# Kernel optimization log

Hardware: AMD Instinct MI355X
Metric: run time of the kernel (lower is better)

## Reference

```python
import jax, jax.numpy as jnp
import numpy as np

B, T, I, H = 64, 512, 1024, 2048


def setup_inputs() -> dict:
    key = jax.random.key(0)
    ks = jax.random.split(key, 6)
    s = 1.0 / np.sqrt(H).astype(np.float32)
    return {
        "input": jax.random.normal(ks[0], (B, T, I), jnp.float32),
        "internal": jax.random.normal(ks[1], (B, T), jnp.float32) * 0.1,
        "w_ih": jax.random.uniform(ks[2], (H, I), jnp.float32, -s, s),
        "w_hh": jax.random.uniform(ks[3], (H, H), jnp.float32, -s, s),
        "b_ih": jax.random.uniform(ks[4], (H,), jnp.float32, -s, s),
        "b_hh": jax.random.uniform(ks[5], (H,), jnp.float32, -s, s),
        "h0": jnp.zeros((1, B, H), jnp.float32),
        "trunc": 64,
    }


def reference(input, internal, w_ih, w_hh, b_ih, b_hh, h0, trunc):
    # input: [B, T, I]; internal: [B, T] scalar-per-step drive; h0: [1, B, H]
    Tlen = input.shape[1]
    # Hoist the input projection out of the recurrence (same math, one big GEMM).
    x_proj = jnp.einsum('bti,hi->bth', input, w_ih) + b_ih  # [B, T, H]
    # Truncated-BPTT boundaries: state is detached when i % trunc == 0.
    detach_mask = (jnp.arange(Tlen) % trunc) == 0  # [T] bool

    def step(h, xs):
        xp, noise, m = xs  # xp: [B, H], noise: [B], m: scalar bool
        # detach state at truncation boundary (no-op in forward pass)
        h = jnp.where(m, jax.lax.stop_gradient(h), h)
        h_new = jnp.tanh(xp + noise[:, None] + h @ w_hh.T + b_hh)
        return h_new, h_new

    h_last, outs = jax.lax.scan(
        step, h0[0], (x_proj.transpose(1, 0, 2), internal.T, detach_mask))
    # outputs: [B, T, H], final state: [1, B, H]
    return outs.transpose(1, 0, 2), h_last[None]
```

## Files before the change

kernel.cpp:

```cpp
#include <hip/hip_runtime.h>
#include <hip/hip_bf16.h>
#include <math.h>

#define Bb 64
#define Tt 512
#define Ii 1024
#define Hh 2048
#define NBLK 128

typedef __attribute__((ext_vector_type(8))) short bf16x8;
typedef __attribute__((ext_vector_type(8))) unsigned short ushort8;
typedef __attribute__((ext_vector_type(4))) float f32x4;

__device__ __forceinline__ unsigned short f2bf(float x) {
    unsigned int u = __float_as_uint(x);
    unsigned int r = u + 0x7fffu + ((u >> 16) & 1u);
    return (unsigned short)(r >> 16);
}

__global__ __launch_bounds__(256) void cvt_kernel(
    const float* __restrict__ src, unsigned short* __restrict__ dst)
{
    const int i = (blockIdx.x * 256 + threadIdx.x) * 4;
    float4 v = *(const float4*)(src + i);
    ushort4 o;
    o.x = f2bf(v.x); o.y = f2bf(v.y); o.z = f2bf(v.z); o.w = f2bf(v.w);
    *(ushort4*)(dst + i) = o;
}

__global__ void init_flags(unsigned int* flags) {
    if (threadIdx.x < NBLK + 2) flags[threadIdx.x] = 0u;
}

__global__ __launch_bounds__(256, 2) void xproj_kernel(
    const float* __restrict__ A,
    const unsigned short* __restrict__ Wbf,
    const float* __restrict__ bias,
    float* __restrict__ out)
{
    __shared__ unsigned short As[128 * 40];
    __shared__ unsigned short Bs[128 * 40];

    const int tid  = threadIdx.x;
    const int lane = tid & 63;
    const int wid  = tid >> 6;
    const int wm   = wid & 1;
    const int wn   = wid >> 1;
    const int rlo  = lane & 15;
    const int khi  = lane >> 4;

    const int m0 = blockIdx.y * 128;
    const int n0 = blockIdx.x * 128;

    f32x4 acc[4][4];
    #pragma unroll
    for (int i = 0; i < 4; ++i)
        #pragma unroll
        for (int j = 0; j < 4; ++j) acc[i][j] = (f32x4)0.f;

    for (int k0 = 0; k0 < Ii; k0 += 32) {
        #pragma unroll
        for (int p = 0; p < 4; ++p) {
            const int flat = p * 256 + tid;
            const int row  = flat >> 3;
            const int c4   = flat & 7;
            float4 v = *(const float4*)(A + (size_t)(m0 + row) * Ii + k0 + c4 * 4);
            ushort4 o;
            o.x = f2bf(v.x); o.y = f2bf(v.y); o.z = f2bf(v.z); o.w = f2bf(v.w);
            *(ushort4*)(As + row * 40 + c4 * 4) = o;
        }
        #pragma unroll
        for (int p = 0; p < 2; ++p) {
            const int flat = p * 256 + tid;
            const int row  = flat >> 2;
            const int c8   = flat & 3;
            ushort8 v = *(const ushort8*)(Wbf + (size_t)(n0 + row) * Ii + k0 + c8 * 8);
            *(ushort8*)(Bs + row * 40 + c8 * 8) = v;
        }
        __syncthreads();

        bf16x8 af[4], bfr[4];
        #pragma unroll
        for (int i = 0; i < 4; ++i)
            af[i] = *(const bf16x8*)(As + (wm * 64 + i * 16 + rlo) * 40 + khi * 8);
        #pragma unroll
        for (int j = 0; j < 4; ++j)
            bfr[j] = *(const bf16x8*)(Bs + (wn * 64 + j * 16 + rlo) * 40 + khi * 8);
        #pragma unroll
        for (int i = 0; i < 4; ++i)
            #pragma unroll
            for (int j = 0; j < 4; ++j)
                acc[i][j] = __builtin_amdgcn_mfma_f32_16x16x32_bf16(
                    af[i], bfr[j], acc[i][j], 0, 0, 0);
        __syncthreads();
    }

    #pragma unroll
    for (int j = 0; j < 4; ++j) {
        const int col = n0 + wn * 64 + j * 16 + rlo;
        const float bj = bias[col];
        #pragma unroll
        for (int i = 0; i < 4; ++i) {
            #pragma unroll
            for (int r = 0; r < 4; ++r) {
                const int m = m0 + wm * 64 + i * 16 + khi * 4 + r;
                out[(size_t)m * Hh + col] = acc[i][j][r] + bj;
            }
        }
    }
}

#define LD_FRAG(dst, base, OFF)                                               \
    asm volatile("global_load_dwordx4 %0, %1, off offset:" OFF " sc0 sc1"     \
                 : "=v"(dst) : "v"(base))

#define LD_FRAG_C(dst, base, OFF)                                             \
    asm volatile("global_load_dwordx4 %0, %1, off offset:" OFF                \
                 : "=v"(dst) : "v"(base))

#define DRAIN16(a)                                                            \
    asm volatile("s_waitcnt vmcnt(0)"                                         \
                 : "+v"(a[0][0]), "+v"(a[0][1]), "+v"(a[0][2]), "+v"(a[0][3]),\
                   "+v"(a[0][4]), "+v"(a[0][5]), "+v"(a[0][6]), "+v"(a[0][7]),\
                   "+v"(a[1][0]), "+v"(a[1][1]), "+v"(a[1][2]), "+v"(a[1][3]),\
                   "+v"(a[1][4]), "+v"(a[1][5]), "+v"(a[1][6]), "+v"(a[1][7]) \
                 :: "memory");                                                \
    __builtin_amdgcn_sched_barrier(0)

#define RAW_BARRIER()                                                         \
    asm volatile("s_waitcnt lgkmcnt(0)\n\ts_barrier" ::: "memory")

__global__ __launch_bounds__(512, 2) void rnn_persistent(
    const unsigned short* __restrict__ w_bf,
    unsigned short* __restrict__ h_bf,
    const float* __restrict__ b_hh,
    const float* __restrict__ internal,
    float* __restrict__ out,
    unsigned int* __restrict__ flags)
{
    __shared__ f32x4 red4[8 * 256];

    const int tid  = threadIdx.x;
    const int lane = tid & 63;
    const int wid  = tid >> 6;
    const int rlo  = lane & 15;
    const int khi  = lane >> 4;
    const int blk  = blockIdx.x;
    const int rh   = blk & 1;
    const int cg   = blk >> 1;

    bf16x8 wf[2][8];
    {
        const unsigned short* w0 =
            w_bf + (size_t)(cg * 32 + rlo) * Hh + wid * 256 + khi * 8;
        const unsigned short* w1 = w0 + (size_t)16 * Hh;
        LD_FRAG_C(wf[0][0], w0, "0");   LD_FRAG_C(wf[0][1], w0, "64");
        LD_FRAG_C(wf[0][2], w0, "128"); LD_FRAG_C(wf[0][3], w0, "192");
        LD_FRAG_C(wf[0][4], w0, "256"); LD_FRAG_C(wf[0][5], w0, "320");
        LD_FRAG_C(wf[0][6], w0, "384"); LD_FRAG_C(wf[0][7], w0, "448");
        LD_FRAG_C(wf[1][0], w1, "0");   LD_FRAG_C(wf[1][1], w1, "64");
        LD_FRAG_C(wf[1][2], w1, "128"); LD_FRAG_C(wf[1][3], w1, "192");
        LD_FRAG_C(wf[1][4], w1, "256"); LD_FRAG_C(wf[1][5], w1, "320");
        LD_FRAG_C(wf[1][6], w1, "384"); LD_FRAG_C(wf[1][7], w1, "448");
        DRAIN16(wf);
    }

    const int em    = (tid >> 6) & 1;
    const int ent   = (tid >> 7) & 1;
    const int odd   = lane & 1;
    const int clloc = (ent * 16 + rlo) & ~1;
    const int cl    = cg * 32 + clloc;
    const int rAl   = em * 16 + khi * 4 + 2 * odd;
    const int rAg   = rh * 32 + rAl;
    const int rBg   = rAg + 1;
    const float2 bh2 = (tid < 256) ? *(const float2*)(b_hh + cl)
                                   : make_float2(0.f, 0.f);

    float2 xpA = make_float2(0.f, 0.f), xpB = make_float2(0.f, 0.f);
    float  nzA = 0.f, nzB = 0.f;
    if (tid < 256) {
        xpA = *(const float2*)(out + ((size_t)rAg * Tt + 0) * Hh + cl);
        xpB = *(const float2*)(out + ((size_t)rBg * Tt + 0) * Hh + cl);
        nzA = internal[rAg * Tt + 0];
        nzB = internal[rBg * Tt + 0];
    }
    float2 gA_d = make_float2(0.f, 0.f), gB_d = make_float2(0.f, 0.f);

    for (int t = 0; t < Tt; ++t) {
        const bool last = (t == Tt - 1);
        const unsigned short* h_cur = h_bf + (size_t)(t & 1) * Bb * Hh;
        unsigned short*       h_nxt = h_bf + (size_t)((t + 1) & 1) * Bb * Hh;

        const unsigned short* am0 =
            h_cur + (size_t)(rh * 32 + rlo) * Hh + wid * 256 + khi * 8;
        const unsigned short* am1 = am0 + (size_t)16 * Hh;

        bf16x8 a[2][8];
        LD_FRAG(a[0][0], am0, "0");   LD_FRAG(a[0][1], am0, "64");
        LD_FRAG(a[0][2], am0, "128"); LD_FRAG(a[0][3], am0, "192");
        LD_FRAG(a[0][4], am0, "256"); LD_FRAG(a[0][5], am0, "320");
        LD_FRAG(a[0][6], am0, "384"); LD_FRAG(a[0][7], am0, "448");
        LD_FRAG(a[1][0], am1, "0");   LD_FRAG(a[1][1], am1, "64");
        LD_FRAG(a[1][2], am1, "128"); LD_FRAG(a[1][3], am1, "192");
        LD_FRAG(a[1][4], am1, "256"); LD_FRAG(a[1][5], am1, "320");
        LD_FRAG(a[1][6], am1, "384"); LD_FRAG(a[1][7], am1, "448");

        if (tid < 256 && t > 0) {
            *(float2*)(out + ((size_t)rAg * Tt + (t - 1)) * Hh + cl) = gA_d;
            *(float2*)(out + ((size_t)rBg * Tt + (t - 1)) * Hh + cl) = gB_d;
        }

        DRAIN16(a);

        f32x4 acc[2][2];
        #pragma unroll
        for (int m = 0; m < 2; ++m)
            #pragma unroll
            for (int nt = 0; nt < 2; ++nt) acc[m][nt] = (f32x4)0.f;
        #pragma unroll
        for (int kk = 0; kk < 8; ++kk)
            #pragma unroll
            for (int m = 0; m < 2; ++m)
                #pragma unroll
                for (int nt = 0; nt < 2; ++nt)
                    acc[m][nt] = __builtin_amdgcn_mfma_f32_16x16x32_bf16(
                        a[m][kk], wf[nt][kk], acc[m][nt], 0, 0, 0);

        #pragma unroll
        for (int nt = 0; nt < 2; ++nt)
            #pragma unroll
            for (int m = 0; m < 2; ++m)
                red4[wid * 256 + (nt * 2 + m) * 64 + lane] = acc[m][nt];
        RAW_BARRIER();

        if (tid < 256) {
            f32x4 s4 = (f32x4)0.f;
            #pragma unroll
            for (int ks = 0; ks < 8; ++ks)
                s4 += red4[ks * 256 + tid];

            f32x4 o4;
            #pragma unroll
            for (int i = 0; i < 4; ++i)
                o4[i] = __shfl_xor(s4[i], 1, 64);

            const float sA_lo = odd ? o4[2] : s4[0];
            const float sA_hi = odd ? s4[2] : o4[0];
            const float sB_lo = odd ? o4[3] : s4[1];
            const float sB_hi = odd ? s4[3] : o4[1];

            float2 gA, gB;
            gA.x = tanhf(xpA.x + nzA + bh2.x + sA_lo);
            gA.y = tanhf(xpA.y + nzA + bh2.y + sA_hi);
            gB.x = tanhf(xpB.x + nzB + bh2.x + sB_lo);
            gB.y = tanhf(xpB.y + nzB + bh2.y + sB_hi);

            const unsigned int hpA =
                (unsigned int)f2bf(gA.x) | ((unsigned int)f2bf(gA.y) << 16);
            const unsigned int hpB =
                (unsigned int)f2bf(gB.x) | ((unsigned int)f2bf(gB.y) << 16);
            __hip_atomic_store((unsigned int*)h_nxt + ((size_t)rAg * Hh + cl) / 2,
                               hpA, __ATOMIC_RELAXED, __HIP_MEMORY_SCOPE_AGENT);
            __hip_atomic_store((unsigned int*)h_nxt + ((size_t)rBg * Hh + cl) / 2,
                               hpB, __ATOMIC_RELAXED, __HIP_MEMORY_SCOPE_AGENT);

            if (last) {
                *(float2*)(out + ((size_t)rAg * Tt + t) * Hh + cl) = gA;
                *(float2*)(out + ((size_t)rBg * Tt + t) * Hh + cl) = gB;
                float* tail = out + (size_t)Bb * Tt * Hh;
                *(float2*)(tail + (size_t)rAg * Hh + cl) = gA;
                *(float2*)(tail + (size_t)rBg * Hh + cl) = gB;
            } else {
                gA_d = gA; gB_d = gB;
            }
        }
        if (last) break;

        asm volatile("s_waitcnt vmcnt(0)" ::: "memory");

        if (tid < 256) {
            xpA = *(const float2*)(out + ((size_t)rAg * Tt + t + 1) * Hh + cl);
            xpB = *(const float2*)(out + ((size_t)rBg * Tt + t + 1) * Hh + cl);
            nzA = internal[rAg * Tt + t + 1];
            nzB = internal[rBg * Tt + t + 1];
        }

        RAW_BARRIER();

        if (tid == 0)
            __hip_atomic_store(flags + blk, (unsigned int)(t + 1),
                               __ATOMIC_RELAXED, __HIP_MEMORY_SCOPE_AGENT);

        const unsigned int tgt = (unsigned int)(t + 1);
        if (blk < 2 && wid == 7) {
            while (true) {
                unsigned int f = __hip_atomic_load(
                    flags + lane * 2 + blk, __ATOMIC_RELAXED,
                    __HIP_MEMORY_SCOPE_AGENT);
                if (__all(f >= tgt)) break;
                __builtin_amdgcn_s_sleep(1);
            }
            if (lane == 0)
                __hip_atomic_store(flags + NBLK + blk, tgt, __ATOMIC_RELAXED,
                                   __HIP_MEMORY_SCOPE_AGENT);
        } else if (wid == 7) {
            while (__hip_atomic_load(flags + NBLK + rh, __ATOMIC_RELAXED,
                                     __HIP_MEMORY_SCOPE_AGENT) < tgt)
                __builtin_amdgcn_s_sleep(1);
        }
        RAW_BARRIER();
    }
}

extern "C" void kernel_launch(void* const* d_in, const int* in_sizes, int n_in,
                              void* d_out, int out_size, void* d_ws, size_t ws_size,
                              hipStream_t stream) {
    const float* input    = (const float*)d_in[0];
    const float* internal = (const float*)d_in[1];
    const float* w_ih     = (const float*)d_in[2];
    const float* w_hh     = (const float*)d_in[3];
    const float* b_ih     = (const float*)d_in[4];
    const float* b_hh     = (const float*)d_in[5];
    const float* h0       = (const float*)d_in[6];
    float* out = (float*)d_out;

    unsigned short* w_hh_bf = (unsigned short*)d_ws;
    unsigned short* w_ih_bf = w_hh_bf + (size_t)Hh * Hh;
    unsigned short* h_bf    = w_ih_bf + (size_t)Hh * Ii;
    unsigned int*   flags   = (unsigned int*)(h_bf + (size_t)2 * Bb * Hh);

    hipLaunchKernelGGL(init_flags, dim3(1), dim3(256), 0, stream, flags);
    hipLaunchKernelGGL(cvt_kernel, dim3((Hh * Hh) / 1024), dim3(256), 0, stream,
                       w_hh, w_hh_bf);
    hipLaunchKernelGGL(cvt_kernel, dim3((Hh * Ii) / 1024), dim3(256), 0, stream,
                       w_ih, w_ih_bf);
    hipLaunchKernelGGL(cvt_kernel, dim3((Bb * Hh) / 1024), dim3(256), 0, stream,
                       h0, h_bf);

    dim3 g1(Hh / 128, (Bb * Tt) / 128);
    hipLaunchKernelGGL(xproj_kernel, g1, dim3(256), 0, stream,
                       input, w_ih_bf, b_ih, out);

    void* args[] = {(void*)&w_hh_bf, (void*)&h_bf, (void*)&b_hh,
                    (void*)&internal, (void*)&out, (void*)&flags};
    hipLaunchCooperativeKernel((void*)rnn_persistent, dim3(NBLK), dim3(512),
                               args, 0, stream);
}
```

Measured before the change: 3.957 ms.

## Use per-wave arrival flags and replicated root flags in grid barrier

Each of the four compute waves now publishes its own step flag as soon as its h stores have drained, instead of the block waiting at a barrier and thread 0 publishing one flag. The two aggregator blocks poll four flags per lane with cache-bypassing loads and publish the release to 16 padded root copies. Pollers spread across those copies to cut contention on a single cache line. This drops one block-wide barrier per step and overlaps the next-step xproj loads with the signalling. The trade-offs are more flag traffic and a larger flag array that must be zeroed at launch.

New measurement: 3.809 ms. 3.8% less time.

```diff
diff --git a/kernel.cpp b/kernel.cpp
--- a/kernel.cpp
+++ b/kernel.cpp
@@ -28,8 +28,8 @@
     *(ushort4*)(dst + i) = o;
 }
 
-__global__ void init_flags(unsigned int* flags) {
-    if (threadIdx.x < NBLK + 2) flags[threadIdx.x] = 0u;
+__global__ __launch_bounds__(1024) void init_flags(unsigned int* flags) {
+    flags[threadIdx.x] = 0u;
 }
 
 __global__ __launch_bounds__(256, 2) void xproj_kernel(
@@ -186,6 +186,11 @@
     }
     float2 gA_d = make_float2(0.f, 0.f), gB_d = make_float2(0.f, 0.f);
 
+    unsigned int* myflag   = flags + blk * 4 + wid;
+    unsigned int* aggbase  = flags + 8 * lane + 4 * rh;
+    unsigned int* rootst   = flags + 512 + (rh * 16 + lane) * 16;
+    unsigned int* rootpoll = flags + 512 + (rh * 16 + ((blk >> 1) & 15)) * 16;
+
     for (int t = 0; t < Tt; ++t) {
         const bool last = (t == Tt - 1);
         const unsigned short* h_cur = h_bf + (size_t)(t & 1) * Bb * Hh;
@@ -272,39 +277,45 @@
                 *(float2*)(tail + (size_t)rBg * Hh + cl) = gB;
             } else {
                 gA_d = gA; gB_d = gB;
+
+                asm volatile("s_waitcnt vmcnt(0)" ::: "memory");
+                if (lane == 0)
+                    __hip_atomic_store(myflag, (unsigned int)(t + 1),
+                                       __ATOMIC_RELAXED,
+                                       __HIP_MEMORY_SCOPE_AGENT);
+
+                xpA = *(const float2*)(out + ((size_t)rAg * Tt + t + 1) * Hh + cl);
+                xpB = *(const float2*)(out + ((size_t)rBg * Tt + t + 1) * Hh + cl);
+                nzA = internal[rAg * Tt + t + 1];
+                nzB = internal[rBg * Tt + t + 1];
             }
         }
         if (last) break;
-
-        asm volatile("s_waitcnt vmcnt(0)" ::: "memory");
-
-        if (tid < 256) {
-            xpA = *(const float2*)(out + ((size_t)rAg * Tt + t + 1) * Hh + cl);
-            xpB = *(const float2*)(out + ((size_t)rBg * Tt + t + 1) * Hh + cl);
-            nzA = internal[rAg * Tt + t + 1];
-            nzB = internal[rBg * Tt + t + 1];
-        }
-
-        RAW_BARRIER();
-
-        if (tid == 0)
-            __hip_atomic_store(flags + blk, (unsigned int)(t + 1),
-                               __ATOMIC_RELAXED, __HIP_MEMORY_SCOPE_AGENT);
 
         const unsigned int tgt = (unsigned int)(t + 1);
         if (blk < 2 && wid == 7) {
+            unsigned int f0, f1, f2, f3;
             while (true) {
-                unsigned int f = __hip_atomic_load(
-                    flags + lane * 2 + blk, __ATOMIC_RELAXED,
-                    __HIP_MEMORY_SCOPE_AGENT);
-                if (__all(f >= tgt)) break;
+                asm volatile("global_load_dword %0, %1, off sc0 sc1"
+                             : "=v"(f0) : "v"(aggbase));
+                asm volatile("global_load_dword %0, %1, off offset:4 sc0 sc1"
+                             : "=v"(f1) : "v"(aggbase));
+                asm volatile("global_load_dword %0, %1, off offset:8 sc0 sc1"
+                             : "=v"(f2) : "v"(aggbase));
+                asm volatile("global_load_dword %0, %1, off offset:12 sc0 sc1"
+                             : "=v"(f3) : "v"(aggbase));
+                asm volatile("s_waitcnt vmcnt(0)"
+                             : "+v"(f0), "+v"(f1), "+v"(f2), "+v"(f3)
+                             :: "memory");
+                if (__all(f0 >= tgt && f1 >= tgt && f2 >= tgt && f3 >= tgt))
+                    break;
                 __builtin_amdgcn_s_sleep(1);
             }
-            if (lane == 0)
-                __hip_atomic_store(flags + NBLK + blk, tgt, __ATOMIC_RELAXED,
+            if (lane < 16)
+                __hip_atomic_store(rootst, tgt, __ATOMIC_RELAXED,
                                    __HIP_MEMORY_SCOPE_AGENT);
         } else if (wid == 7) {
-            while (__hip_atomic_load(flags + NBLK + rh, __ATOMIC_RELAXED,
+            while (__hip_atomic_load(rootpoll, __ATOMIC_RELAXED,
                                      __HIP_MEMORY_SCOPE_AGENT) < tgt)
                 __builtin_amdgcn_s_sleep(1);
         }
@@ -329,7 +340,7 @@
     unsigned short* h_bf    = w_ih_bf + (size_t)Hh * Ii;
     unsigned int*   flags   = (unsigned int*)(h_bf + (size_t)2 * Bb * Hh);
 
-    hipLaunchKernelGGL(init_flags, dim3(1), dim3(256), 0, stream, flags);
+    hipLaunchKernelGGL(init_flags, dim3(1), dim3(1024), 0, stream, flags);
     hipLaunchKernelGGL(cvt_kernel, dim3((Hh * Hh) / 1024), dim3(256), 0, stream,
                        w_hh, w_hh_bf);
     hipLaunchKernelGGL(cvt_kernel, dim3((Hh * Ii) / 1024), dim3(256), 0, stream,
```

## Replace two-level grid barrier with per-wave flag dataflow sync

Applied to the files above, without the earlier changes.

Drops the centralized two-level grid barrier (block flags aggregated by two leader blocks) and replaces it with per-wave flags. Each wave polls only the 32 producer flags covering its K slice of h before loading it. The reduction buffer is double-buffered by step parity, which removes the trailing block barrier. The intent is to cut barrier latency and let blocks proceed as soon as their specific inputs are ready. The cost is more polling traffic and subtler memory-ordering correctness.

After: 4.002 ms. Within noise of the previous version (+1.1%).

```diff
diff --git a/kernel.cpp b/kernel.cpp
--- a/kernel.cpp
+++ b/kernel.cpp
@@ -28,8 +28,8 @@
     *(ushort4*)(dst + i) = o;
 }
 
-__global__ void init_flags(unsigned int* flags) {
-    if (threadIdx.x < NBLK + 2) flags[threadIdx.x] = 0u;
+__global__ __launch_bounds__(512) void init_flags(unsigned int* flags) {
+    flags[threadIdx.x] = 0u;
 }
 
 __global__ __launch_bounds__(256, 2) void xproj_kernel(
@@ -138,7 +138,7 @@
     float* __restrict__ out,
     unsigned int* __restrict__ flags)
 {
-    __shared__ f32x4 red4[8 * 256];
+    __shared__ f32x4 red4[2][8 * 256];
 
     const int tid  = threadIdx.x;
     const int lane = tid & 63;
@@ -186,10 +186,23 @@
     }
     float2 gA_d = make_float2(0.f, 0.f), gB_d = make_float2(0.f, 0.f);
 
+    unsigned int*       myflag = flags + rh * 256 + cg * 4 + wid;
+    const unsigned int* pollf  = flags + rh * 256 + wid * 32 + (lane & 31);
+
     for (int t = 0; t < Tt; ++t) {
         const bool last = (t == Tt - 1);
         const unsigned short* h_cur = h_bf + (size_t)(t & 1) * Bb * Hh;
         unsigned short*       h_nxt = h_bf + (size_t)((t + 1) & 1) * Bb * Hh;
+
+        if (t) {
+            const unsigned int tgt = (unsigned int)t;
+            while (true) {
+                unsigned int f = __hip_atomic_load(
+                    pollf, __ATOMIC_RELAXED, __HIP_MEMORY_SCOPE_AGENT);
+                if (__all(f >= tgt)) break;
+                __builtin_amdgcn_s_sleep(1);
+            }
+        }
 
         const unsigned short* am0 =
             h_cur + (size_t)(rh * 32 + rlo) * Hh + wid * 256 + khi * 8;
@@ -226,18 +239,19 @@
                     acc[m][nt] = __builtin_amdgcn_mfma_f32_16x16x32_bf16(
                         a[m][kk], wf[nt][kk], acc[m][nt], 0, 0, 0);
 
+        f32x4* rb = red4[t & 1];
         #pragma unroll
         for (int nt = 0; nt < 2; ++nt)
             #pragma unroll
             for (int m = 0; m < 2; ++m)
-                red4[wid * 256 + (nt * 2 + m) * 64 + lane] = acc[m][nt];
+                rb[wid * 256 + (nt * 2 + m) * 64 + lane] = acc[m][nt];
         RAW_BARRIER();
 
         if (tid < 256) {
             f32x4 s4 = (f32x4)0.f;
             #pragma unroll
             for (int ks = 0; ks < 8; ++ks)
-                s4 += red4[ks * 256 + tid];
+                s4 += rb[ks * 256 + tid];
 
             f32x4 o4;
             #pragma unroll
@@ -272,43 +286,19 @@
                 *(float2*)(tail + (size_t)rBg * Hh + cl) = gB;
             } else {
                 gA_d = gA; gB_d = gB;
+
+                asm volatile("s_waitcnt vmcnt(0)" ::: "memory");
+                if (lane == 0)
+                    __hip_atomic_store(myflag, (unsigned int)(t + 1),
+                                       __ATOMIC_RELAXED,
+                                       __HIP_MEMORY_SCOPE_AGENT);
+
+                xpA = *(const float2*)(out + ((size_t)rAg * Tt + t + 1) * Hh + cl);
+                xpB = *(const float2*)(out + ((size_t)rBg * Tt + t + 1) * Hh + cl);
+                nzA = internal[rAg * Tt + t + 1];
+                nzB = internal[rBg * Tt + t + 1];
             }
         }
-        if (last) break;
-
-        asm volatile("s_waitcnt vmcnt(0)" ::: "memory");
-
-        if (tid < 256) {
-            xpA = *(const float2*)(out + ((size_t)rAg * Tt + t + 1) * Hh + cl);
-            xpB = *(const float2*)(out + ((size_t)rBg * Tt + t + 1) * Hh + cl);
-            nzA = internal[rAg * Tt + t + 1];
-            nzB = internal[rBg * Tt + t + 1];
-        }
-
-        RAW_BARRIER();
-
-        if (tid == 0)
-            __hip_atomic_store(flags + blk, (unsigned int)(t + 1),
-                               __ATOMIC_RELAXED, __HIP_MEMORY_SCOPE_AGENT);
-
-        const unsigned int tgt = (unsigned int)(t + 1);
-        if (blk < 2 && wid == 7) {
-            while (true) {
-                unsigned int f = __hip_atomic_load(
-                    flags + lane * 2 + blk, __ATOMIC_RELAXED,
-                    __HIP_MEMORY_SCOPE_AGENT);
-                if (__all(f >= tgt)) break;
-                __builtin_amdgcn_s_sleep(1);
-            }
-            if (lane == 0)
-                __hip_atomic_store(flags + NBLK + blk, tgt, __ATOMIC_RELAXED,
-                                   __HIP_MEMORY_SCOPE_AGENT);
-        } else if (wid == 7) {
-            while (__hip_atomic_load(flags + NBLK + rh, __ATOMIC_RELAXED,
-                                     __HIP_MEMORY_SCOPE_AGENT) < tgt)
-                __builtin_amdgcn_s_sleep(1);
-        }
-        RAW_BARRIER();
     }
 }
 
@@ -329,7 +319,7 @@
     unsigned short* h_bf    = w_ih_bf + (size_t)Hh * Ii;
     unsigned int*   flags   = (unsigned int*)(h_bf + (size_t)2 * Bb * Hh);
 
-    hipLaunchKernelGGL(init_flags, dim3(1), dim3(256), 0, stream, flags);
+    hipLaunchKernelGGL(init_flags, dim3(1), dim3(512), 0, stream, flags);
     hipLaunchKernelGGL(cvt_kernel, dim3((Hh * Hh) / 1024), dim3(256), 0, stream,
                        w_hh, w_hh_bf);
     hipLaunchKernelGGL(cvt_kernel, dim3((Hh * Ii) / 1024), dim3(256), 0, stream,
```
